# Kernel optimization log

Measured on AMD Instinct MI355X. Metric: run time of the kernel, lower is better.

## Reference

```python
import jax, jax.numpy as jnp
import numpy as np

S, D, H = 2048, 1024, 16
DH = D // H
EPS = 1e-5


def setup_inputs() -> dict:
    key = jax.random.key(0)
    ks = jax.random.split(key, 6)
    scale = 0.02
    return {
        "inputs": jax.random.normal(ks[0], (S, D), dtype=jnp.float32),
        "ln_w": jnp.ones((D,), dtype=jnp.float32),
        "ln_b": jnp.zeros((D,), dtype=jnp.float32),
        "Wq": jax.random.normal(ks[1], (D, D), dtype=jnp.float32) * scale,
        "Wk": jax.random.normal(ks[2], (D, D), dtype=jnp.float32) * scale,
        "Wv": jax.random.normal(ks[3], (D, D), dtype=jnp.float32) * scale,
        "Wo": jax.random.normal(ks[4], (D, D), dtype=jnp.float32) * scale,
    }


def reference(inputs, ln_w, ln_b, Wq, Wk, Wv, Wo):
    # Pre-LayerNorm (per token), matching eqx.nn.LayerNorm (eps=1e-5)
    mu = jnp.mean(inputs, axis=-1, keepdims=True)
    var = jnp.var(inputs, axis=-1, keepdims=True)
    x = (inputs - mu) / jnp.sqrt(var + EPS) * ln_w + ln_b  # [S, D]

    # QKV projections (eqx Linear: y = W @ x, no bias) -> [S, H, DH]
    q = (x @ Wq.T).reshape(S, H, DH)
    k = (x @ Wk.T).reshape(S, H, DH)
    v = (x @ Wv.T).reshape(S, H, DH)

    # Scaled dot-product attention; softmax forced to full precision
    scores = jnp.einsum("shd,thd->hst", q, k) / jnp.sqrt(jnp.asarray(DH, x.dtype))
    attn = jax.nn.softmax(scores.astype(jnp.float32), axis=-1).astype(x.dtype)
    # (dropout is identity in inference mode)
    ctx = jnp.einsum("hst,thd->shd", attn, v).reshape(S, D)

    out = ctx @ Wo.T  # output projection
    # outer dropout is identity in inference mode; residual add
    return out + inputs
```

## Files before the change

kernel.cpp:

```cpp
#include <hip/hip_runtime.h>
#include <cstdint>
#include <cstddef>

typedef unsigned short u16;
typedef unsigned int u32;
typedef __attribute__((ext_vector_type(8))) short bf16x8;
typedef __attribute__((ext_vector_type(4))) short bf16x4;
typedef __attribute__((ext_vector_type(4))) float f32x4;
typedef __attribute__((ext_vector_type(4))) unsigned short u16x4;

#if __has_builtin(__builtin_amdgcn_mfma_f32_16x16x16bf16_1k)
#define MFMA16(a, b, c) __builtin_amdgcn_mfma_f32_16x16x16bf16_1k(a, b, c, 0, 0, 0)
#else
static __device__ __forceinline__ f32x4 mfma16_asm(bf16x4 a, bf16x4 b, f32x4 c) {
  asm volatile("v_mfma_f32_16x16x16_bf16 %0, %1, %2, %0\n\ts_nop 4"
               : "+v"(c) : "v"(a), "v"(b));
  return c;
}
#define MFMA16(a, b, c) mfma16_asm(a, b, c)
#endif

__device__ __forceinline__ u16 f2b(float f) {
  union { float f; unsigned u; } un; un.f = f;
  unsigned u = un.u;
  return (u16)((u + 0x7fffu + ((u >> 16) & 1u)) >> 16);
}

__device__ __forceinline__ u32 pkbf(float a, float b) {
  union { float f; u32 u; } ua, ub; ua.f = a; ub.f = b;
  return ((ua.u + 0x8000u) >> 16) | (((ub.u + 0x8000u) >> 16) << 16);
}

__device__ __forceinline__ void gload_lds16(const u16* g, u16* l) {
  __builtin_amdgcn_global_load_lds(
      (const __attribute__((address_space(1))) void*)g,
      (__attribute__((address_space(3))) void*)l, 16, 0, 0);
}

__device__ __forceinline__ void gemm128x64(
    const u16* __restrict__ A, const u16* __restrict__ B,
    u16* smA, u16* smB, int bm, int bn,
    float* outf, u16* outb, const float* __restrict__ resid, int ostride)
{
  const int tid = threadIdx.x;
  const int wave = tid >> 6, lane = tid & 63;
  const int quad = lane >> 4, l16 = lane & 15;
  const int wm = wave >> 1, wn = wave & 1;

  f32x4 acc[4][2];
  const f32x4 zero4 = {0.f, 0.f, 0.f, 0.f};
#pragma unroll
  for (int i = 0; i < 4; i++)
#pragma unroll
    for (int j = 0; j < 2; j++) acc[i][j] = zero4;

  for (int k0 = 0; k0 < 1024; k0 += 32) {
#pragma unroll
    for (int r = 0; r < 2; r++) {
      const int c = r * 256 + wave * 64 + lane;
      gload_lds16(A + (size_t)(bm * 128 + (c >> 2)) * 1024 + k0 + (c & 3) * 8,
                  smA + (size_t)(r * 256 + wave * 64) * 8);
    }
    {
      const int c = wave * 64 + lane;
      gload_lds16(B + (size_t)(bn * 64 + (c >> 2)) * 1024 + k0 + (c & 3) * 8,
                  smB + (size_t)(wave * 64) * 8);
    }
    __syncthreads();
    bf16x8 afr[4], bfr[2];
#pragma unroll
    for (int t = 0; t < 4; t++)
      afr[t] = *(const bf16x8*)(smA + (wm * 64 + t * 16 + l16) * 32 + quad * 8);
#pragma unroll
    for (int t = 0; t < 2; t++)
      bfr[t] = *(const bf16x8*)(smB + (wn * 32 + t * 16 + l16) * 32 + quad * 8);
#pragma unroll
    for (int mt = 0; mt < 4; mt++)
#pragma unroll
      for (int nt = 0; nt < 2; nt++)
        acc[mt][nt] = __builtin_amdgcn_mfma_f32_16x16x32_bf16(afr[mt], bfr[nt], acc[mt][nt], 0, 0, 0);
    __syncthreads();
  }
#pragma unroll
  for (int mt = 0; mt < 4; mt++)
#pragma unroll
    for (int nt = 0; nt < 2; nt++)
#pragma unroll
      for (int r = 0; r < 4; r++) {
        const int row = bm * 128 + wm * 64 + mt * 16 + quad * 4 + r;
        const int col = bn * 64 + wn * 32 + nt * 16 + l16;
        if (outb) outb[(size_t)row * ostride + col] = f2b(acc[mt][nt][r]);
        else outf[(size_t)row * ostride + col] =
                 acc[mt][nt][r] + resid[(size_t)row * ostride + col];
      }
}

__global__ __launch_bounds__(256, 3) void proj_k(
    const u16* __restrict__ xb, const u16* __restrict__ Wb,
    u16* __restrict__ qkbuf, u16* __restrict__ vTb)
{
  __shared__ u16 smA[128 * 32];
  __shared__ u16 smB[64 * 32];
  int b = blockIdx.x;
  const u16 *A, *B; u16* o; int bm, bn;
  if (b < 512) {
    A = xb; B = Wb; o = qkbuf; bm = b >> 5; bn = b & 31;
  } else {
    b -= 512;
    A = Wb + (size_t)2 * (1 << 20); B = xb; o = vTb; bm = b >> 5; bn = b & 31;
  }
  gemm128x64(A, B, smA, smB, bm, bn, nullptr, o, nullptr, 2048);
}

__global__ __launch_bounds__(256, 3) void out_k(
    const u16* __restrict__ ctxb, const u16* __restrict__ Wob,
    float* __restrict__ out, const float* __restrict__ x)
{
  __shared__ u16 smA[128 * 32];
  __shared__ u16 smB[64 * 32];
  gemm128x64(ctxb, Wob, smA, smB, blockIdx.y, blockIdx.x, out, nullptr, x, 1024);
}

__global__ __launch_bounds__(256) void pre_k(
    const float* __restrict__ x, const float* __restrict__ lnw, const float* __restrict__ lnb,
    const float* __restrict__ w0, const float* __restrict__ w1,
    const float* __restrict__ w2, const float* __restrict__ w3,
    u16* __restrict__ xb, u16* __restrict__ Wb)
{
  const int b = blockIdx.x;
  const int tid = threadIdx.x;
  if (b < 2048) {
    const int s = b;
    const float4 v = ((const float4*)(x + (size_t)s * 1024))[tid];
    float sum = v.x + v.y + v.z + v.w;
    float sq  = v.x * v.x + v.y * v.y + v.z * v.z + v.w * v.w;
#pragma unroll
    for (int off = 32; off >= 1; off >>= 1) {
      sum += __shfl_down(sum, off);
      sq  += __shfl_down(sq, off);
    }
    __shared__ float sS[4], sQ[4];
    const int wave = tid >> 6, lane = tid & 63;
    if (lane == 0) { sS[wave] = sum; sQ[wave] = sq; }
    __syncthreads();
    const float ts = sS[0] + sS[1] + sS[2] + sS[3];
    const float tq = sQ[0] + sQ[1] + sQ[2] + sQ[3];
    const float mu = ts * (1.0f / 1024.0f);
    const float var = tq * (1.0f / 1024.0f) - mu * mu;
    const float rstd = rsqrtf(var + 1e-5f);
    const float4 wv = ((const float4*)lnw)[tid];
    const float4 bv = ((const float4*)lnb)[tid];
    u16x4 o;
    o[0] = f2b((v.x - mu) * rstd * wv.x + bv.x);
    o[1] = f2b((v.y - mu) * rstd * wv.y + bv.y);
    o[2] = f2b((v.z - mu) * rstd * wv.z + bv.z);
    o[3] = f2b((v.w - mu) * rstd * wv.w + bv.w);
    *(u16x4*)(xb + (size_t)s * 1024 + tid * 4) = o;
  } else {
    const unsigned i = (unsigned)(b - 2048) * 1024u + tid * 4u;
    const unsigned NW = 1u << 20;
    const float* src; unsigned loc; float sc;
    if (i < NW)            { src = w0; loc = i;           sc = 0.125f; }
    else if (i < 2u * NW)  { src = w1; loc = i - NW;      sc = 1.0f; }
    else if (i < 3u * NW)  { src = w2; loc = i - 2u * NW; sc = 1.0f; }
    else                   { src = w3; loc = i - 3u * NW; sc = 1.0f; }
    const float4 v = *(const float4*)(src + loc);
    u16x4 r;
    r[0] = f2b(v.x * sc); r[1] = f2b(v.y * sc); r[2] = f2b(v.z * sc); r[3] = f2b(v.w * sc);
    *(u16x4*)(Wb + i) = r;
  }
}

__global__ __launch_bounds__(256, 2) void attn_k(
    const u16* __restrict__ qkbuf,
    const u16* __restrict__ vT,
    u16* __restrict__ ctx)
{
  const int h = blockIdx.y;
  const int q0 = blockIdx.x * 64;
  __shared__ __align__(16) unsigned char arena[65536];
  u16* kvbuf = (u16*)arena;
  const int tid = threadIdx.x;
  const int wave = tid >> 6, lane = tid & 63;
  const int quad = lane >> 4, l16 = lane & 15;
  const int a7 = l16 & 7;
  const u16* kg = qkbuf + 1024;

  bf16x8 qf[4][2];
#pragma unroll
  for (int s = 0; s < 4; s++)
#pragma unroll
    for (int ks = 0; ks < 2; ks++)
      qf[s][ks] = *(const bf16x8*)(qkbuf + (size_t)(q0 + s * 16 + l16) * 2048 + h * 64 + ks * 32 + quad * 8);

  const f32x4 zero4 = {0.f, 0.f, 0.f, 0.f};
  f32x4 Oacc[4][4];
#pragma unroll
  for (int s = 0; s < 4; s++)
#pragma unroll
    for (int dt = 0; dt < 4; dt++) Oacc[s][dt] = zero4;
  float lacc[4] = {0.f, 0.f, 0.f, 0.f};

#define STAGE(T, bf)                                                                     \
  {                                                                                      \
    _Pragma("unroll")                                                                    \
    for (int i = 0; i < 4; i++) {                                                        \
      const int idx = (wave * 4 + i) * 64 + lane;                                        \
      const int kt = idx >> 3, kc = (idx & 7) ^ (kt & 7);                                \
      gload_lds16(kg + (size_t)((T) * 128 + kt) * 2048 + h * 64 + kc * 8,                \
                  kvbuf + (bf) * 16384 + (size_t)(wave * 4 + i) * 512);                  \
      const int vd = idx >> 4, vc = (idx & 15) ^ (vd & 7);                               \
      gload_lds16(vT + (size_t)(h * 64 + vd) * 2048 + (T) * 128 + vc * 8,                \
                  kvbuf + (bf) * 16384 + 8192 + (size_t)(wave * 4 + i) * 512);           \
    }                                                                                    \
  }

  STAGE(0, 0);
  __syncthreads();

  for (int T = 0; T < 16; T++) {
    const int bf = T & 1;
    if (T + 1 < 16) STAGE(T + 1, 1 - bf);
    const u16* kb = kvbuf + bf * 16384;
    const u16* vb = kb + 8192;

    f32x4 st[2][4];
#pragma unroll
    for (int ntl = 0; ntl < 2; ntl++) {
      const int nt = wave * 2 + ntl;
      const u16* kr = kb + (nt * 16 + l16) * 64;
      const bf16x8 ka0 = *(const bf16x8*)(kr + (quad ^ a7) * 8);
      const bf16x8 ka1 = *(const bf16x8*)(kr + ((4 + quad) ^ a7) * 8);
#pragma unroll
      for (int s = 0; s < 4; s++) {
        f32x4 t0 = __builtin_amdgcn_mfma_f32_16x16x32_bf16(ka0, qf[s][0], zero4, 0, 0, 0);
        st[ntl][s] = __builtin_amdgcn_mfma_f32_16x16x32_bf16(ka1, qf[s][1], t0, 0, 0, 0);
      }
    }

    bf16x4 pk[2][4];
#pragma unroll
    for (int ntl = 0; ntl < 2; ntl++)
#pragma unroll
      for (int s = 0; s < 4; s++) {
        const float p0 = __expf(st[ntl][s][0]);
        const float p1 = __expf(st[ntl][s][1]);
        const float p2 = __expf(st[ntl][s][2]);
        const float p3 = __expf(st[ntl][s][3]);
        lacc[s] += (p0 + p1) + (p2 + p3);
        union { u32 u[2]; bf16x4 v; } pp;
        pp.u[0] = pkbf(p0, p1);
        pp.u[1] = pkbf(p2, p3);
        pk[ntl][s] = pp.v;
      }

#pragma unroll
    for (int ntl = 0; ntl < 2; ntl++)
#pragma unroll
      for (int dt = 0; dt < 4; dt++) {
        const bf16x4 bv = *(const bf16x4*)(vb + (dt * 16 + l16) * 128 +
            (((wave * 4 + ntl * 2 + (quad >> 1)) ^ a7) * 8 + (quad & 1) * 4));
#pragma unroll
        for (int s = 0; s < 4; s++)
          Oacc[s][dt] = MFMA16(pk[ntl][s], bv, Oacc[s][dt]);
      }
    __syncthreads();
  }
#undef STAGE

  float* rl = (float*)arena;
#pragma unroll
  for (int s = 0; s < 4; s++) {
    float l = lacc[s];
    l += __shfl_xor(l, 16);
    l += __shfl_xor(l, 32);
    if (quad == 0) rl[wave * 64 + s * 16 + l16] = l;
  }
  __syncthreads();
  const int m = tid >> 2, dg = (tid & 3) * 16;
  const float inv = 1.0f / (rl[m] + rl[64 + m] + rl[128 + m] + rl[192 + m]);
  __syncthreads();

  float* ro = (float*)arena;
#pragma unroll
  for (int s = 0; s < 4; s++)
#pragma unroll
    for (int dt = 0; dt < 4; dt++)
#pragma unroll
      for (int r = 0; r < 4; r++) {
        const int mr = s * 16 + quad * 4 + r;
        const int dc = (dt * 16 + l16) ^ ((mr & 7) << 1);
        ro[wave * 4096 + mr * 64 + dc] = Oacc[s][dt][r];
      }
  __syncthreads();
  u16* dst = ctx + (size_t)(q0 + m) * 1024 + h * 64 + dg;
  const int msw = (m & 7) << 1;
#pragma unroll
  for (int g = 0; g < 4; g++) {
    u16x4 o;
#pragma unroll
    for (int j = 0; j < 4; j++) {
      const int dc = (dg + g * 4 + j) ^ msw;
      const int base = m * 64 + dc;
      const float v = ro[base] + ro[4096 + base] + ro[8192 + base] + ro[12288 + base];
      o[j] = f2b(v * inv);
    }
    *(u16x4*)(dst + g * 4) = o;
  }
}

extern "C" void kernel_launch(void* const* d_in, const int* in_sizes, int n_in,
                              void* d_out, int out_size, void* d_ws, size_t ws_size,
                              hipStream_t stream)
{
  const float* x   = (const float*)d_in[0];
  const float* lnw = (const float*)d_in[1];
  const float* lnb = (const float*)d_in[2];
  const float* Wq  = (const float*)d_in[3];
  const float* Wk  = (const float*)d_in[4];
  const float* Wv  = (const float*)d_in[5];
  const float* Wo  = (const float*)d_in[6];

  u16* ws    = (u16*)d_ws;
  u16* xb    = ws;
  u16* Wb    = xb + (size_t)2048 * 1024;
  u16* qkbuf = Wb + (size_t)4 * 1024 * 1024;
  u16* vTb   = qkbuf + (size_t)2048 * 2048;
  u16* ctxb  = vTb + (size_t)1024 * 2048;

  pre_k<<<6144, 256, 0, stream>>>(x, lnw, lnb, Wq, Wk, Wv, Wo, xb, Wb);
  proj_k<<<768, 256, 0, stream>>>(xb, Wb, qkbuf, vTb);
  attn_k<<<dim3(32, 16), 256, 0, stream>>>(qkbuf, vTb, ctxb);
  out_k<<<dim3(16, 16), 256, 0, stream>>>(ctxb, Wb + (size_t)3 * (1 << 20), (float*)d_out, x);
}
```

Before: 153.3 us.

## Double-buffer GEMM K-loop, remap blocks for XCD locality, use exp2 softmax

The projection and output GEMMs now load K tiles of 64 into double-buffered LDS, prefetching the next tile while MFMAs run on the current one, so there is one barrier per 64 of K instead of two per 32. Block indices in the projection, attention and output kernels are remapped so that neighbouring tiles land on the same chiplet (XCD), which should improve L2 reuse. The Q weights are pre-scaled by log2(e)/8 so the softmax can use the hardware exp2 instead of __expf. The cost is more LDS per block (48 KB), which may lower occupancy below the requested 3 blocks per CU.

```diff
diff --git a/kernel.cpp b/kernel.cpp
--- a/kernel.cpp
+++ b/kernel.cpp
@@ -20,6 +20,12 @@
 #define MFMA16(a, b, c) mfma16_asm(a, b, c)
 #endif
 
+#if __has_builtin(__builtin_amdgcn_exp2f)
+#define EXP2(x) __builtin_amdgcn_exp2f(x)
+#else
+#define EXP2(x) exp2f(x)
+#endif
+
 __device__ __forceinline__ u16 f2b(float f) {
   union { float f; unsigned u; } un; un.f = f;
   unsigned u = un.u;
@@ -54,33 +60,51 @@
 #pragma unroll
     for (int j = 0; j < 2; j++) acc[i][j] = zero4;
 
-  for (int k0 = 0; k0 < 1024; k0 += 32) {
-#pragma unroll
-    for (int r = 0; r < 2; r++) {
-      const int c = r * 256 + wave * 64 + lane;
-      gload_lds16(A + (size_t)(bm * 128 + (c >> 2)) * 1024 + k0 + (c & 3) * 8,
-                  smA + (size_t)(r * 256 + wave * 64) * 8);
-    }
-    {
-      const int c = wave * 64 + lane;
-      gload_lds16(B + (size_t)(bn * 64 + (c >> 2)) * 1024 + k0 + (c & 3) * 8,
-                  smB + (size_t)(wave * 64) * 8);
+  const u16* Ab = A + (size_t)(bm * 128) * 1024;
+  const u16* Bb = B + (size_t)(bn * 64) * 1024;
+
+#define PSTAGE(buf, k0)                                                          \
+  {                                                                              \
+    _Pragma("unroll")                                                            \
+    for (int ks = 0; ks < 2; ks++) {                                             \
+      _Pragma("unroll")                                                          \
+      for (int r = 0; r < 2; r++) {                                              \
+        const int c = r * 256 + wave * 64 + lane;                                \
+        gload_lds16(Ab + (size_t)(c >> 2) * 1024 + (k0) + ks * 32 + (c & 3) * 8, \
+                    smA + (buf) * 8192 + ks * 4096 + (size_t)(r * 256 + wave * 64) * 8); \
+      }                                                                          \
+      const int c2 = wave * 64 + lane;                                           \
+      gload_lds16(Bb + (size_t)(c2 >> 2) * 1024 + (k0) + ks * 32 + (c2 & 3) * 8, \
+                  smB + (buf) * 4096 + ks * 2048 + (size_t)(wave * 64) * 8);     \
+    }                                                                            \
+  }
+
+  PSTAGE(0, 0);
+  __syncthreads();
+  for (int t = 0; t < 16; t++) {
+    const int cur = t & 1;
+    if (t < 15) PSTAGE(cur ^ 1, (t + 1) * 64);
+    const u16* sa = smA + cur * 8192;
+    const u16* sb = smB + cur * 4096;
+#pragma unroll
+    for (int ks = 0; ks < 2; ks++) {
+      bf16x8 afr[4], bfr[2];
+#pragma unroll
+      for (int tt = 0; tt < 4; tt++)
+        afr[tt] = *(const bf16x8*)(sa + ks * 4096 + (wm * 64 + tt * 16 + l16) * 32 + quad * 8);
+#pragma unroll
+      for (int tt = 0; tt < 2; tt++)
+        bfr[tt] = *(const bf16x8*)(sb + ks * 2048 + (wn * 32 + tt * 16 + l16) * 32 + quad * 8);
+#pragma unroll
+      for (int mt = 0; mt < 4; mt++)
+#pragma unroll
+        for (int nt = 0; nt < 2; nt++)
+          acc[mt][nt] = __builtin_amdgcn_mfma_f32_16x16x32_bf16(afr[mt], bfr[nt], acc[mt][nt], 0, 0, 0);
     }
     __syncthreads();
-    bf16x8 afr[4], bfr[2];
-#pragma unroll
-    for (int t = 0; t < 4; t++)
-      afr[t] = *(const bf16x8*)(smA + (wm * 64 + t * 16 + l16) * 32 + quad * 8);
-#pragma unroll
-    for (int t = 0; t < 2; t++)
-      bfr[t] = *(const bf16x8*)(smB + (wn * 32 + t * 16 + l16) * 32 + quad * 8);
-#pragma unroll
-    for (int mt = 0; mt < 4; mt++)
-#pragma unroll
-      for (int nt = 0; nt < 2; nt++)
-        acc[mt][nt] = __builtin_amdgcn_mfma_f32_16x16x32_bf16(afr[mt], bfr[nt], acc[mt][nt], 0, 0, 0);
-    __syncthreads();
-  }
+  }
+#undef PSTAGE
+
 #pragma unroll
   for (int mt = 0; mt < 4; mt++)
 #pragma unroll
@@ -99,15 +123,21 @@
     const u16* __restrict__ xb, const u16* __restrict__ Wb,
     u16* __restrict__ qkbuf, u16* __restrict__ vTb)
 {
-  __shared__ u16 smA[128 * 32];
-  __shared__ u16 smB[64 * 32];
+  __shared__ u16 smA[2 * 128 * 64];
+  __shared__ u16 smB[2 * 64 * 64];
   int b = blockIdx.x;
   const u16 *A, *B; u16* o; int bm, bn;
   if (b < 512) {
-    A = xb; B = Wb; o = qkbuf; bm = b >> 5; bn = b & 31;
+    const int c = b & 7, i = b >> 3;
+    bm = ((c >> 2) << 3) | (i & 7);
+    bn = ((c & 3) << 3) | (i >> 3);
+    A = xb; B = Wb; o = qkbuf;
   } else {
     b -= 512;
-    A = Wb + (size_t)2 * (1 << 20); B = xb; o = vTb; bm = b >> 5; bn = b & 31;
+    const int c = b & 7, i = b >> 3;
+    bm = i & 7;
+    bn = (c << 2) | (i >> 3);
+    A = Wb + (size_t)2 * (1 << 20); B = xb; o = vTb;
   }
   gemm128x64(A, B, smA, smB, bm, bn, nullptr, o, nullptr, 2048);
 }
@@ -116,9 +146,13 @@
     const u16* __restrict__ ctxb, const u16* __restrict__ Wob,
     float* __restrict__ out, const float* __restrict__ x)
 {
-  __shared__ u16 smA[128 * 32];
-  __shared__ u16 smB[64 * 32];
-  gemm128x64(ctxb, Wob, smA, smB, blockIdx.y, blockIdx.x, out, nullptr, x, 1024);
+  __shared__ u16 smA[2 * 128 * 64];
+  __shared__ u16 smB[2 * 64 * 64];
+  const int b = blockIdx.x;
+  const int c = b & 7, i = b >> 3;
+  const int bm = ((c >> 2) << 3) | (i & 7);
+  const int bn = ((c & 3) << 2) | (i >> 3);
+  gemm128x64(ctxb, Wob, smA, smB, bm, bn, out, nullptr, x, 1024);
 }
 
 __global__ __launch_bounds__(256) void pre_k(
@@ -160,7 +194,7 @@
     const unsigned i = (unsigned)(b - 2048) * 1024u + tid * 4u;
     const unsigned NW = 1u << 20;
     const float* src; unsigned loc; float sc;
-    if (i < NW)            { src = w0; loc = i;           sc = 0.125f; }
+    if (i < NW)            { src = w0; loc = i;           sc = 0.18033688f; }
     else if (i < 2u * NW)  { src = w1; loc = i - NW;      sc = 1.0f; }
     else if (i < 3u * NW)  { src = w2; loc = i - 2u * NW; sc = 1.0f; }
     else                   { src = w3; loc = i - 3u * NW; sc = 1.0f; }
@@ -176,8 +210,10 @@
     const u16* __restrict__ vT,
     u16* __restrict__ ctx)
 {
-  const int h = blockIdx.y;
-  const int q0 = blockIdx.x * 64;
+  const int bid = blockIdx.x;
+  const int work = (bid & 7) * 64 + (bid >> 3);
+  const int h = work >> 5;
+  const int q0 = (work & 31) * 64;
   __shared__ __align__(16) unsigned char arena[65536];
   u16* kvbuf = (u16*)arena;
   const int tid = threadIdx.x;
@@ -243,10 +279,10 @@
     for (int ntl = 0; ntl < 2; ntl++)
 #pragma unroll
       for (int s = 0; s < 4; s++) {
-        const float p0 = __expf(st[ntl][s][0]);
-        const float p1 = __expf(st[ntl][s][1]);
-        const float p2 = __expf(st[ntl][s][2]);
-        const float p3 = __expf(st[ntl][s][3]);
+        const float p0 = EXP2(st[ntl][s][0]);
+        const float p1 = EXP2(st[ntl][s][1]);
+        const float p2 = EXP2(st[ntl][s][2]);
+        const float p3 = EXP2(st[ntl][s][3]);
         lacc[s] += (p0 + p1) + (p2 + p3);
         union { u32 u[2]; bf16x4 v; } pp;
         pp.u[0] = pkbf(p0, p1);
@@ -330,6 +366,6 @@
 
   pre_k<<<6144, 256, 0, stream>>>(x, lnw, lnb, Wq, Wk, Wv, Wo, xb, Wb);
   proj_k<<<768, 256, 0, stream>>>(xb, Wb, qkbuf, vTb);
-  attn_k<<<dim3(32, 16), 256, 0, stream>>>(qkbuf, vTb, ctxb);
-  out_k<<<dim3(16, 16), 256, 0, stream>>>(ctxb, Wb + (size_t)3 * (1 << 20), (float*)d_out, x);
-}
+  attn_k<<<512, 256, 0, stream>>>(qkbuf, vTb, ctxb);
+  out_k<<<256, 256, 0, stream>>>(ctxb, Wb + (size_t)3 * (1 << 20), (float*)d_out, x);
+}
```

After: 153.8 us. Within noise of the previous version (+0.3%).
